# Kernel optimization log

Hardware: AMD Instinct MI355X
Metric: run time of the kernel (lower is better)

Reference implementation:

```python
import jax, jax.numpy as jnp
import numpy as np

PH = PW = 33   # patch size of base_net
IMH = IMW = 24 # output map size (one base_net eval per pixel)
SLOPE = 0.01   # LeakyReLU negative slope used in base AnomalyNet


def _conv(x, w, b):
    y = jax.lax.conv_general_dilated(x, w, (1, 1), 'VALID',
                                     dimension_numbers=('NCHW', 'OIHW', 'NCHW'))
    return y + b[None, :, None, None]


def _pool2(x):
    return jax.lax.reduce_window(x, -jnp.inf, jax.lax.max,
                                 (1, 1, 2, 2), (1, 1, 2, 2), 'VALID')


def _base_net(p, c1w, c1b, c2w, c2b, c3w, c3b, c4w, c4b, c5w, c5b, dw, db):
    lr = lambda h: jax.nn.leaky_relu(h, SLOPE)
    h = _pool2(lr(_conv(p, c1w, c1b)))   # (N,128,14,14)
    h = _pool2(lr(_conv(h, c2w, c2b)))   # (N,128,5,5)
    h = lr(_conv(h, c3w, c3b))           # (N,128,1,1)
    h = lr(_conv(h, c4w, c4b))           # (N,256,1,1)
    h = lr(_conv(h, c5w, c5b))           # (N,128,1,1)
    h = h.reshape(h.shape[0], -1)        # (N,128)
    return h @ dw.T + db                 # (N,512)


def setup_inputs() -> dict:
    key = jax.random.key(0)
    ks = jax.random.split(key, 8)
    he = lambda k, shape, fan_in: (jax.random.normal(k, shape, jnp.float32)
                                   * np.float32(np.sqrt(2.0 / fan_in)))
    z = lambda n: jnp.zeros((n,), jnp.float32)
    return {
        'x':   jax.random.normal(ks[0], (1, 3, IMH, IMW), jnp.float32),
        'c1w': he(ks[1], (128, 3, 5, 5), 3 * 25),   'c1b': z(128),
        'c2w': he(ks[2], (128, 128, 5, 5), 128 * 25), 'c2b': z(128),
        'c3w': he(ks[3], (128, 128, 5, 5), 128 * 25), 'c3b': z(128),
        'c4w': he(ks[4], (256, 128, 1, 1), 128),      'c4b': z(256),
        'c5w': he(ks[5], (128, 256, 1, 1), 256),      'c5b': z(128),
        'dw':  he(ks[6], (512, 128), 128),            'db': z(512),
    }


def reference(x, c1w, c1b, c2w, c2b, c3w, c3b, c4w, c4b, c5w, c5b, dw, db):
    B, C = x.shape[0], x.shape[1]
    pady, padx = PH - 1, PW - 1
    # multiPoolPrepare: zero-pad so every output pixel has a full PHxPW patch
    xp = jnp.pad(x, ((0, 0), (0, 0),
                     (pady // 2, pady - pady // 2),
                     (padx // 2, padx - padx // 2)))
    # all overlapping PHxPW patches, one per output pixel (replaces the i,j loops)
    patches = jax.lax.conv_general_dilated_patches(
        xp, (PH, PW), (1, 1), 'VALID',
        dimension_numbers=('NCHW', 'OIHW', 'NCHW'))  # (B, C*PH*PW, IMH, IMW)
    patches = patches.reshape(B, C, PH, PW, IMH, IMW)
    patches = patches.transpose(0, 4, 5, 1, 2, 3).reshape(B * IMH * IMW, C, PH, PW)
    feats = _base_net(patches, c1w, c1b, c2w, c2b, c3w, c3b,
                      c4w, c4b, c5w, c5b, dw, db)      # (B*IMH*IMW, 512)
    return feats.reshape(B, IMH, IMW, -1).transpose(0, 3, 1, 2)  # (B,512,IMH,IMW)
```

## Files before the change

kernel.cpp:

```cpp
#include <hip/hip_runtime.h>

#define SLOPE 0.01f

typedef __attribute__((ext_vector_type(8))) short short8;
typedef __attribute__((ext_vector_type(4))) float f32x4;

__device__ __forceinline__ float lrelu(float v) { return v >= 0.f ? v : SLOPE * v; }

__device__ __forceinline__ unsigned short f2bf(float f) {
    union { float f; unsigned int u; } v; v.f = f;
    unsigned int r = v.u + 0x7fffu + ((v.u >> 16) & 1u);
    return (unsigned short)(r >> 16);
}
__device__ __forceinline__ float bf2f(unsigned short h) {
    union { unsigned int u; float f; } v; v.u = ((unsigned int)h) << 16;
    return v.f;
}

__device__ __forceinline__ int swz(int oc, int k, int Kdiv32) {
    return (((oc >> 4) * Kdiv32 + (k >> 5)) * 64 + ((k >> 3) & 3) * 16 + (oc & 15)) * 8 + (k & 7);
}


__global__ __launch_bounds__(256) void k_front(const float* __restrict__ x,
                                               const float* __restrict__ c1w,
                                               const float* __restrict__ c1b,
                                               const float* __restrict__ c2w,
                                               const float* __restrict__ c3w,
                                               const float* __restrict__ c4w,
                                               const float* __restrict__ c5w,
                                               const float* __restrict__ dw,
                                               unsigned short* __restrict__ P2,
                                               unsigned short* __restrict__ W2s,
                                               unsigned short* __restrict__ W3s,
                                               unsigned short* __restrict__ C4Bs,
                                               unsigned short* __restrict__ C5Bs,
                                               unsigned short* __restrict__ DWBs) {
    __shared__ float smem[9600];
    int bid = blockIdx.x, tid = threadIdx.x;

    if (bid < 1250) {
        for (int idx = tid; idx < 9600; idx += 256) smem[idx] = c1w[idx];
        __syncthreads();

        int t = bid * 256 + tid;
        int ic = t & 127;
        int rest = t >> 7;
        int B = rest % 25;
        int A = (rest / 25) % 25;
        int ph = rest / 625;
        int py = ph >> 1, px = ph & 1;
        int r0 = 2 * A + py, s0 = 2 * B + px;

        float a00 = 0.f, a01 = 0.f, a10 = 0.f, a11 = 0.f;
        const float* lw = smem + ic * 75;
        for (int c = 0; c < 3; ++c) {
            const float* xc = x + c * 576;
            const float* lwc = lw + c * 25;
#pragma unroll
            for (int ky = 0; ky < 5; ++ky) {
                int iy = r0 + ky - 16;
                bool v0 = (iy >= 0) && (iy < 24);
                bool v1 = (iy + 1 >= 0) && (iy + 1 < 24);
                if (!v0 && !v1) continue;
#pragma unroll
                for (int kx = 0; kx < 5; ++kx) {
                    int ix = s0 + kx - 16;
                    float w = lwc[ky * 5 + kx];
                    bool u0 = (ix >= 0) && (ix < 24);
                    bool u1 = (ix + 1 >= 0) && (ix + 1 < 24);
                    float x00 = (v0 && u0) ? xc[iy * 24 + ix] : 0.f;
                    float x01 = (v0 && u1) ? xc[iy * 24 + ix + 1] : 0.f;
                    float x10 = (v1 && u0) ? xc[(iy + 1) * 24 + ix] : 0.f;
                    float x11 = (v1 && u1) ? xc[(iy + 1) * 24 + ix + 1] : 0.f;
                    a00 += x00 * w; a01 += x01 * w; a10 += x10 * w; a11 += x11 * w;
                }
            }
        }
        float mx = fmaxf(fmaxf(a00, a01), fmaxf(a10, a11));
        P2[t] = f2bf(lrelu(c1b[ic] + mx));
    } else if (bid < 1506) {
        int wbid = bid - 1250;
        int oc = wbid & 127;
        const float* src = (wbid < 128) ? (c2w + oc * 3200) : (c3w + oc * 3200);
        unsigned short* dst = (wbid < 128) ? W2s : W3s;
        for (int idx = tid; idx < 3200; idx += 256) smem[idx] = src[idx];
        __syncthreads();
        for (int idx = tid; idx < 3200; idx += 256) {
            int ic = idx & 127, kpos = idx >> 7;
            dst[swz(oc, kpos * 128 + ic, 100)] = f2bf(smem[ic * 25 + kpos]);
        }
    } else {
        int e = (bid - 1506) * 256 + tid;
        if (e < 32768) {
            int oc = e >> 7, k = e & 127;
            C4Bs[swz(oc, k, 4)] = f2bf(c4w[e]);
        } else if (e < 65536) {
            int e2 = e - 32768;
            int oc = e2 >> 8, k = e2 & 255;
            C5Bs[swz(oc, k, 8)] = f2bf(c5w[e2]);
        } else {
            int e2 = e - 65536;
            int oc = e2 >> 7, k = e2 & 127;
            DWBs[swz(oc, k, 4)] = f2bf(dw[e2]);
        }
    }
}

__global__ __launch_bounds__(256) void k_conv2(const unsigned short* __restrict__ P2,
                                               const unsigned short* __restrict__ W2s,
                                               const float* __restrict__ bias,
                                               unsigned short* __restrict__ Z2) {
    int bid = blockIdx.x;
    int ph = bid / 42;
    int rem = bid % 42;
    int A = rem >> 1;
    int oh = rem & 1;
    int tid = threadIdx.x, lane = tid & 63, wid = tid >> 6;
    int m = lane & 15, bq = lane >> 4;
    int oc0 = oh * 64 + wid * 16;
    int t = oh * 4 + wid;
    const unsigned short* wbase = W2s + (t * 100 * 64 + lane) * 8;
    const unsigned short* pbase = P2 + ((ph * 25 + A) * 25) * 128 + 8 * bq;
    f32x4 acc0 = {0.f, 0.f, 0.f, 0.f}, acc1 = {0.f, 0.f, 0.f, 0.f};
    for (int kpos = 0; kpos < 25; ++kpos) {
        int ky = kpos / 5, kx = kpos % 5;
        const unsigned short* wp = wbase + kpos * 4 * 512;
        const unsigned short* p0 = pbase + (ky * 25 + m + kx) * 128;
        const unsigned short* p1 = p0 + 5 * 128;
#pragma unroll
        for (int cc = 0; cc < 4; ++cc) {
            short8 a  = *(const short8*)(wp + cc * 512);
            short8 b0 = *(const short8*)(p0 + cc * 32);
            short8 b1 = *(const short8*)(p1 + cc * 32);
            acc0 = __builtin_amdgcn_mfma_f32_16x16x32_bf16(a, b0, acc0, 0, 0, 0);
            acc1 = __builtin_amdgcn_mfma_f32_16x16x32_bf16(a, b1, acc1, 0, 0, 0);
        }
    }
    int ocb = oc0 + 4 * bq;
    float b0v = bias[ocb], b1v = bias[ocb + 1], b2v = bias[ocb + 2], b3v = bias[ocb + 3];
    unsigned short* zrow = Z2 + ((ph * 21 + A) * 21) * 128 + ocb;
    {
        ushort4 pk;
        pk.x = f2bf(lrelu(acc0.x + b0v));
        pk.y = f2bf(lrelu(acc0.y + b1v));
        pk.z = f2bf(lrelu(acc0.z + b2v));
        pk.w = f2bf(lrelu(acc0.w + b3v));
        *(ushort4*)(zrow + m * 128) = pk;
    }
    if (m >= 11) {
        ushort4 pk;
        pk.x = f2bf(lrelu(acc1.x + b0v));
        pk.y = f2bf(lrelu(acc1.y + b1v));
        pk.z = f2bf(lrelu(acc1.z + b2v));
        pk.w = f2bf(lrelu(acc1.w + b3v));
        *(ushort4*)(zrow + (m + 5) * 128) = pk;
    }
}

__global__ __launch_bounds__(256) void k_pool2(const unsigned short* __restrict__ Z2,
                                               unsigned short* __restrict__ Q2) {
    int t = blockIdx.x * 256 + threadIdx.x;
    int ic = t & 127;
    int rest = t >> 7;
    int D = rest % 10;
    int C = (rest / 10) % 10;
    int qph = rest / 100;
    int iq = qph >> 2, jq = qph & 3;
    int ph1 = (iq & 1) * 2 + (jq & 1);
    int py2 = iq >> 1, px2 = jq >> 1;
    int r0 = 2 * C + py2, s0 = 2 * D + px2;
    const unsigned short* z00 = Z2 + ((ph1 * 21 + r0) * 21 + s0) * 128 + ic;
    float m0 = fmaxf(bf2f(z00[0]), bf2f(z00[128]));
    float m1 = fmaxf(bf2f(z00[21 * 128]), bf2f(z00[22 * 128]));
    Q2[t] = f2bf(fmaxf(m0, m1));
}

__global__ __launch_bounds__(512) void k_tail3(const unsigned short* __restrict__ Q2,
                                               const unsigned short* __restrict__ W3s,
                                               const float* __restrict__ c3b,
                                               const unsigned short* __restrict__ C4Bs,
                                               const float* __restrict__ c4b,
                                               const unsigned short* __restrict__ C5Bs,
                                               const float* __restrict__ c5b,
                                               const unsigned short* __restrict__ DWBs,
                                               const float* __restrict__ db,
                                               float* __restrict__ out) {
    __shared__ unsigned short h3bf[16 * 136];
    __shared__ unsigned short h4bf[16 * 264];
    __shared__ unsigned short h5bf[16 * 136];

    int bid = blockIdx.x, tid = threadIdx.x;
    int n0 = bid * 16;
    int lane = tid & 63, w = tid >> 6;
    int m = lane & 15, bq = lane >> 4;

    {
        int p = n0 + m;
        int i = p / 24, j = p % 24;
        int qph = (i & 3) * 4 + (j & 3);
        int C0 = i >> 2, D0 = j >> 2;
        const unsigned short* qbase = Q2 + qph * 12800 + (C0 * 10 + D0) * 128 + 8 * bq;
        const unsigned short* wbase = W3s + (w * 100 * 64 + lane) * 8;
        f32x4 acc = {0.f, 0.f, 0.f, 0.f};
        for (int kpos = 0; kpos < 25; ++kpos) {
            int e = kpos / 5, f = kpos % 5;
            const unsigned short* qp = qbase + (e * 10 + f) * 128;
            const unsigned short* wp = wbase + kpos * 4 * 512;
#pragma unroll
            for (int cc = 0; cc < 4; ++cc) {
                short8 a = *(const short8*)(wp + cc * 512);
                short8 b = *(const short8*)(qp + cc * 32);
                acc = __builtin_amdgcn_mfma_f32_16x16x32_bf16(a, b, acc, 0, 0, 0);
            }
        }
        int oc = w * 16 + bq * 4;
        float v0 = lrelu(acc.x + c3b[oc + 0]);
        float v1 = lrelu(acc.y + c3b[oc + 1]);
        float v2 = lrelu(acc.z + c3b[oc + 2]);
        float v3 = lrelu(acc.w + c3b[oc + 3]);
        uint2 pk;
        pk.x = (unsigned)f2bf(v0) | ((unsigned)f2bf(v1) << 16);
        pk.y = (unsigned)f2bf(v2) | ((unsigned)f2bf(v3) << 16);
        *(uint2*)(&h3bf[m * 136 + oc]) = pk;
    }
    __syncthreads();

    {
        f32x4 acc[2] = {{0,0,0,0},{0,0,0,0}};
#pragma unroll
        for (int t = 0; t < 2; ++t) {
            const unsigned short* abase = C4Bs + (((w * 2 + t) * 4) * 64 + lane) * 8;
#pragma unroll
            for (int cc = 0; cc < 4; ++cc) {
                short8 a = *(const short8*)(abase + cc * 512);
                short8 b = *(const short8*)(&h3bf[m * 136 + cc * 32 + 8 * bq]);
                acc[t] = __builtin_amdgcn_mfma_f32_16x16x32_bf16(a, b, acc[t], 0, 0, 0);
            }
        }
#pragma unroll
        for (int t = 0; t < 2; ++t) {
            int oc = (w * 2 + t) * 16 + bq * 4;
            float v0 = lrelu(acc[t].x + c4b[oc + 0]);
            float v1 = lrelu(acc[t].y + c4b[oc + 1]);
            float v2 = lrelu(acc[t].z + c4b[oc + 2]);
            float v3 = lrelu(acc[t].w + c4b[oc + 3]);
            uint2 pk;
            pk.x = (unsigned)f2bf(v0) | ((unsigned)f2bf(v1) << 16);
            pk.y = (unsigned)f2bf(v2) | ((unsigned)f2bf(v3) << 16);
            *(uint2*)(&h4bf[m * 264 + oc]) = pk;
        }
    }
    __syncthreads();

    {
        const unsigned short* abase = C5Bs + ((w * 8) * 64 + lane) * 8;
        f32x4 acc = {0.f, 0.f, 0.f, 0.f};
#pragma unroll
        for (int cc = 0; cc < 8; ++cc) {
            short8 a = *(const short8*)(abase + cc * 512);
            short8 b = *(const short8*)(&h4bf[m * 264 + cc * 32 + 8 * bq]);
            acc = __builtin_amdgcn_mfma_f32_16x16x32_bf16(a, b, acc, 0, 0, 0);
        }
        int oc = w * 16 + bq * 4;
        float v0 = lrelu(acc.x + c5b[oc + 0]);
        float v1 = lrelu(acc.y + c5b[oc + 1]);
        float v2 = lrelu(acc.z + c5b[oc + 2]);
        float v3 = lrelu(acc.w + c5b[oc + 3]);
        uint2 pk;
        pk.x = (unsigned)f2bf(v0) | ((unsigned)f2bf(v1) << 16);
        pk.y = (unsigned)f2bf(v2) | ((unsigned)f2bf(v3) << 16);
        *(uint2*)(&h5bf[m * 136 + oc]) = pk;
    }
    __syncthreads();

    {
        f32x4 acc[4] = {{0,0,0,0},{0,0,0,0},{0,0,0,0},{0,0,0,0}};
#pragma unroll
        for (int t = 0; t < 4; ++t) {
            const unsigned short* abase = DWBs + (((w * 4 + t) * 4) * 64 + lane) * 8;
#pragma unroll
            for (int cc = 0; cc < 4; ++cc) {
                short8 a = *(const short8*)(abase + cc * 512);
                short8 b = *(const short8*)(&h5bf[m * 136 + cc * 32 + 8 * bq]);
                acc[t] = __builtin_amdgcn_mfma_f32_16x16x32_bf16(a, b, acc[t], 0, 0, 0);
            }
        }
#pragma unroll
        for (int t = 0; t < 4; ++t) {
            int oc = (w * 4 + t) * 16 + bq * 4;
            out[(oc + 0) * 576 + n0 + m] = acc[t].x + db[oc + 0];
            out[(oc + 1) * 576 + n0 + m] = acc[t].y + db[oc + 1];
            out[(oc + 2) * 576 + n0 + m] = acc[t].z + db[oc + 2];
            out[(oc + 3) * 576 + n0 + m] = acc[t].w + db[oc + 3];
        }
    }
}

extern "C" void kernel_launch(void* const* d_in, const int* in_sizes, int n_in,
                              void* d_out, int out_size, void* d_ws, size_t ws_size,
                              hipStream_t stream) {
    const float* x   = (const float*)d_in[0];
    const float* c1w = (const float*)d_in[1];
    const float* c1b = (const float*)d_in[2];
    const float* c2w = (const float*)d_in[3];
    const float* c2b = (const float*)d_in[4];
    const float* c3w = (const float*)d_in[5];
    const float* c3b = (const float*)d_in[6];
    const float* c4w = (const float*)d_in[7];
    const float* c4b = (const float*)d_in[8];
    const float* c5w = (const float*)d_in[9];
    const float* c5b = (const float*)d_in[10];
    const float* dw  = (const float*)d_in[11];
    const float* db  = (const float*)d_in[12];
    float* out = (float*)d_out;

    float* ws = (float*)d_ws;
    unsigned short* P2   = (unsigned short*)(ws);
    unsigned short* Z2   = (unsigned short*)(ws + 160000);
    unsigned short* W2s  = (unsigned short*)(ws + 272896);
    unsigned short* W3s  = (unsigned short*)(ws + 477696);
    unsigned short* C4Bs = (unsigned short*)(ws + 682496);
    unsigned short* C5Bs = (unsigned short*)(ws + 698880);
    unsigned short* DWBs = (unsigned short*)(ws + 715264);
    unsigned short* Q2   = (unsigned short*)(ws + 748032);

    k_front<<<2018, 256, 0, stream>>>(x, c1w, c1b, c2w, c3w, c4w, c5w, dw,
                                      P2, W2s, W3s, C4Bs, C5Bs, DWBs);
    k_conv2<<<168, 256, 0, stream>>>(P2, W2s, c2b, Z2);
    k_pool2<<<800, 256, 0, stream>>>(Z2, Q2);
    k_tail3<<<36, 512, 0, stream>>>(Q2, W3s, c3b, C4Bs, c4b, C5Bs, c5b, DWBs, db, out);
}
```

Measured before the change: 82.17 us.

## Fuse pool2 into tail kernel, gathering pooled patches into LDS

Removes the separate pool2 kernel and its Q2 global buffer. Each tail block now gathers and max-pools the 25 5x5 positions for its 16 pixels straight from Z2 into a large LDS tile, then runs conv3 from LDS. This saves one launch and one global round trip, but pooling is recomputed across overlapping blocks and the tail kernel uses about 117 KB of LDS with only 36 blocks.

```diff
diff --git a/kernel.cpp b/kernel.cpp
--- a/kernel.cpp
+++ b/kernel.cpp
@@ -15,6 +15,12 @@
 __device__ __forceinline__ float bf2f(unsigned short h) {
     union { unsigned int u; float f; } v; v.u = ((unsigned int)h) << 16;
     return v.f;
+}
+__device__ __forceinline__ unsigned short bfmax4(unsigned short a, unsigned short b,
+                                                 unsigned short c, unsigned short d) {
+    float m = fmaxf(fmaxf(bf2f(a), bf2f(b)), fmaxf(bf2f(c), bf2f(d)));
+    union { float f; unsigned int u; } v; v.f = m;
+    return (unsigned short)(v.u >> 16);
 }
 
 __device__ __forceinline__ int swz(int oc, int k, int Kdiv32) {
@@ -158,55 +164,69 @@
     }
 }
 
-__global__ __launch_bounds__(256) void k_pool2(const unsigned short* __restrict__ Z2,
-                                               unsigned short* __restrict__ Q2) {
-    int t = blockIdx.x * 256 + threadIdx.x;
-    int ic = t & 127;
-    int rest = t >> 7;
-    int D = rest % 10;
-    int C = (rest / 10) % 10;
-    int qph = rest / 100;
-    int iq = qph >> 2, jq = qph & 3;
-    int ph1 = (iq & 1) * 2 + (jq & 1);
-    int py2 = iq >> 1, px2 = jq >> 1;
-    int r0 = 2 * C + py2, s0 = 2 * D + px2;
-    const unsigned short* z00 = Z2 + ((ph1 * 21 + r0) * 21 + s0) * 128 + ic;
-    float m0 = fmaxf(bf2f(z00[0]), bf2f(z00[128]));
-    float m1 = fmaxf(bf2f(z00[21 * 128]), bf2f(z00[22 * 128]));
-    Q2[t] = f2bf(fmaxf(m0, m1));
-}
-
-__global__ __launch_bounds__(512) void k_tail3(const unsigned short* __restrict__ Q2,
-                                               const unsigned short* __restrict__ W3s,
-                                               const float* __restrict__ c3b,
-                                               const unsigned short* __restrict__ C4Bs,
-                                               const float* __restrict__ c4b,
-                                               const unsigned short* __restrict__ C5Bs,
-                                               const float* __restrict__ c5b,
-                                               const unsigned short* __restrict__ DWBs,
-                                               const float* __restrict__ db,
-                                               float* __restrict__ out) {
-    __shared__ unsigned short h3bf[16 * 136];
-    __shared__ unsigned short h4bf[16 * 264];
-    __shared__ unsigned short h5bf[16 * 136];
+#define QSTR 3208
+__global__ __launch_bounds__(512) void k_tail(const unsigned short* __restrict__ Z2,
+                                              const unsigned short* __restrict__ W3s,
+                                              const float* __restrict__ c3b,
+                                              const unsigned short* __restrict__ C4Bs,
+                                              const float* __restrict__ c4b,
+                                              const unsigned short* __restrict__ C5Bs,
+                                              const float* __restrict__ c5b,
+                                              const unsigned short* __restrict__ DWBs,
+                                              const float* __restrict__ db,
+                                              float* __restrict__ out) {
+    __shared__ unsigned short lds[59904];
+    unsigned short* Qw   = lds;
+    unsigned short* h3bf = lds + 16 * QSTR;
+    unsigned short* h4bf = h3bf + 16 * 136;
+    unsigned short* h5bf = h4bf + 16 * 264;
 
     int bid = blockIdx.x, tid = threadIdx.x;
     int n0 = bid * 16;
     int lane = tid & 63, w = tid >> 6;
     int m = lane & 15, bq = lane >> 4;
 
-    {
-        int p = n0 + m;
-        int i = p / 24, j = p % 24;
-        int qph = (i & 3) * 4 + (j & 3);
-        int C0 = i >> 2, D0 = j >> 2;
-        const unsigned short* qbase = Q2 + qph * 12800 + (C0 * 10 + D0) * 128 + 8 * bq;
-        const unsigned short* wbase = W3s + (w * 100 * 64 + lane) * 8;
+    for (int v = tid; v < 6400; v += 512) {
+        int p = v / 400;
+        int rem = v - p * 400;
+        int kpos = rem >> 4;
+        int ic0 = (rem & 15) * 8;
+        int e = kpos / 5, f = kpos % 5;
+        int n = n0 + p, i = n / 24, j = n % 24;
+        int ph1 = (i & 1) * 2 + (j & 1);
+        int C = (i >> 2) + e, D = (j >> 2) + f;
+        int r0 = 2 * C + ((i >> 1) & 1), s0 = 2 * D + ((j >> 1) & 1);
+        const unsigned short* z = Z2 + ((ph1 * 21 + r0) * 21 + s0) * 128 + ic0;
+        ushort4 za0 = *(const ushort4*)(z);
+        ushort4 za1 = *(const ushort4*)(z + 4);
+        ushort4 zb0 = *(const ushort4*)(z + 128);
+        ushort4 zb1 = *(const ushort4*)(z + 132);
+        ushort4 zc0 = *(const ushort4*)(z + 21 * 128);
+        ushort4 zc1 = *(const ushort4*)(z + 21 * 128 + 4);
+        ushort4 zd0 = *(const ushort4*)(z + 22 * 128);
+        ushort4 zd1 = *(const ushort4*)(z + 22 * 128 + 4);
+        ushort4 r0v, r1v;
+        r0v.x = bfmax4(za0.x, zb0.x, zc0.x, zd0.x);
+        r0v.y = bfmax4(za0.y, zb0.y, zc0.y, zd0.y);
+        r0v.z = bfmax4(za0.z, zb0.z, zc0.z, zd0.z);
+        r0v.w = bfmax4(za0.w, zb0.w, zc0.w, zd0.w);
+        r1v.x = bfmax4(za1.x, zb1.x, zc1.x, zd1.x);
+        r1v.y = bfmax4(za1.y, zb1.y, zc1.y, zd1.y);
+        r1v.z = bfmax4(za1.z, zb1.z, zc1.z, zd1.z);
+        r1v.w = bfmax4(za1.w, zb1.w, zc1.w, zd1.w);
+        unsigned short* dst = Qw + p * QSTR + rem * 8;
+        *(ushort4*)(dst) = r0v;
+        *(ushort4*)(dst + 4) = r1v;
+    }
+    __syncthreads();
+
+    {
+        const unsigned short* qb = Qw + m * QSTR + 8 * bq;
+        const unsigned short* wbase = W3s + (w * 6400 + lane) * 8;
         f32x4 acc = {0.f, 0.f, 0.f, 0.f};
         for (int kpos = 0; kpos < 25; ++kpos) {
-            int e = kpos / 5, f = kpos % 5;
-            const unsigned short* qp = qbase + (e * 10 + f) * 128;
-            const unsigned short* wp = wbase + kpos * 4 * 512;
+            const unsigned short* qp = qb + kpos * 128;
+            const unsigned short* wp = wbase + kpos * 2048;
 #pragma unroll
             for (int cc = 0; cc < 4; ++cc) {
                 short8 a = *(const short8*)(wp + cc * 512);
@@ -215,13 +235,9 @@
             }
         }
         int oc = w * 16 + bq * 4;
-        float v0 = lrelu(acc.x + c3b[oc + 0]);
-        float v1 = lrelu(acc.y + c3b[oc + 1]);
-        float v2 = lrelu(acc.z + c3b[oc + 2]);
-        float v3 = lrelu(acc.w + c3b[oc + 3]);
         uint2 pk;
-        pk.x = (unsigned)f2bf(v0) | ((unsigned)f2bf(v1) << 16);
-        pk.y = (unsigned)f2bf(v2) | ((unsigned)f2bf(v3) << 16);
+        pk.x = (unsigned)f2bf(lrelu(acc.x + c3b[oc])) | ((unsigned)f2bf(lrelu(acc.y + c3b[oc + 1])) << 16);
+        pk.y = (unsigned)f2bf(lrelu(acc.z + c3b[oc + 2])) | ((unsigned)f2bf(lrelu(acc.w + c3b[oc + 3])) << 16);
         *(uint2*)(&h3bf[m * 136 + oc]) = pk;
     }
     __syncthreads();
@@ -230,7 +246,7 @@
         f32x4 acc[2] = {{0,0,0,0},{0,0,0,0}};
 #pragma unroll
         for (int t = 0; t < 2; ++t) {
-            const unsigned short* abase = C4Bs + (((w * 2 + t) * 4) * 64 + lane) * 8;
+            const unsigned short* abase = C4Bs + ((w * 2 + t) * 4 * 64 + lane) * 8;
 #pragma unroll
             for (int cc = 0; cc < 4; ++cc) {
                 short8 a = *(const short8*)(abase + cc * 512);
@@ -241,20 +257,16 @@
 #pragma unroll
         for (int t = 0; t < 2; ++t) {
             int oc = (w * 2 + t) * 16 + bq * 4;
-            float v0 = lrelu(acc[t].x + c4b[oc + 0]);
-            float v1 = lrelu(acc[t].y + c4b[oc + 1]);
-            float v2 = lrelu(acc[t].z + c4b[oc + 2]);
-            float v3 = lrelu(acc[t].w + c4b[oc + 3]);
             uint2 pk;
-            pk.x = (unsigned)f2bf(v0) | ((unsigned)f2bf(v1) << 16);
-            pk.y = (unsigned)f2bf(v2) | ((unsigned)f2bf(v3) << 16);
+            pk.x = (unsigned)f2bf(lrelu(acc[t].x + c4b[oc])) | ((unsigned)f2bf(lrelu(acc[t].y + c4b[oc + 1])) << 16);
+            pk.y = (unsigned)f2bf(lrelu(acc[t].z + c4b[oc + 2])) | ((unsigned)f2bf(lrelu(acc[t].w + c4b[oc + 3])) << 16);
             *(uint2*)(&h4bf[m * 264 + oc]) = pk;
         }
     }
     __syncthreads();
 
     {
-        const unsigned short* abase = C5Bs + ((w * 8) * 64 + lane) * 8;
+        const unsigned short* abase = C5Bs + (w * 8 * 64 + lane) * 8;
         f32x4 acc = {0.f, 0.f, 0.f, 0.f};
 #pragma unroll
         for (int cc = 0; cc < 8; ++cc) {
@@ -263,13 +275,9 @@
             acc = __builtin_amdgcn_mfma_f32_16x16x32_bf16(a, b, acc, 0, 0, 0);
         }
         int oc = w * 16 + bq * 4;
-        float v0 = lrelu(acc.x + c5b[oc + 0]);
-        float v1 = lrelu(acc.y + c5b[oc + 1]);
-        float v2 = lrelu(acc.z + c5b[oc + 2]);
-        float v3 = lrelu(acc.w + c5b[oc + 3]);
         uint2 pk;
-        pk.x = (unsigned)f2bf(v0) | ((unsigned)f2bf(v1) << 16);
-        pk.y = (unsigned)f2bf(v2) | ((unsigned)f2bf(v3) << 16);
+        pk.x = (unsigned)f2bf(lrelu(acc.x + c5b[oc])) | ((unsigned)f2bf(lrelu(acc.y + c5b[oc + 1])) << 16);
+        pk.y = (unsigned)f2bf(lrelu(acc.z + c5b[oc + 2])) | ((unsigned)f2bf(lrelu(acc.w + c5b[oc + 3])) << 16);
         *(uint2*)(&h5bf[m * 136 + oc]) = pk;
     }
     __syncthreads();
@@ -278,7 +286,7 @@
         f32x4 acc[4] = {{0,0,0,0},{0,0,0,0},{0,0,0,0},{0,0,0,0}};
 #pragma unroll
         for (int t = 0; t < 4; ++t) {
-            const unsigned short* abase = DWBs + (((w * 4 + t) * 4) * 64 + lane) * 8;
+            const unsigned short* abase = DWBs + ((w * 4 + t) * 4 * 64 + lane) * 8;
 #pragma unroll
             for (int cc = 0; cc < 4; ++cc) {
                 short8 a = *(const short8*)(abase + cc * 512);
@@ -323,11 +331,9 @@
     unsigned short* C4Bs = (unsigned short*)(ws + 682496);
     unsigned short* C5Bs = (unsigned short*)(ws + 698880);
     unsigned short* DWBs = (unsigned short*)(ws + 715264);
-    unsigned short* Q2   = (unsigned short*)(ws + 748032);
 
     k_front<<<2018, 256, 0, stream>>>(x, c1w, c1b, c2w, c3w, c4w, c5w, dw,
                                       P2, W2s, W3s, C4Bs, C5Bs, DWBs);
     k_conv2<<<168, 256, 0, stream>>>(P2, W2s, c2b, Z2);
-    k_pool2<<<800, 256, 0, stream>>>(Z2, Q2);
-    k_tail3<<<36, 512, 0, stream>>>(Q2, W3s, c3b, C4Bs, c4b, C5Bs, c5b, DWBs, db, out);
-}
+    k_tail<<<36, 512, 0, stream>>>(Z2, W3s, c3b, C4Bs, c4b, C5Bs, c5b, DWBs, db, out);
+}
```

Result: faster. 66.97 us (median of 2 runs) (-18.5%).
